# Kernel optimization log

Measured on AMD Instinct MI355X. Metric: run time of the kernel, lower is better.

Reference implementation:

```python
import jax, jax.numpy as jnp
import numpy as np

G = 200000
M = 9600000

def setup_inputs() -> dict:
    key = jax.random.key(0)
    k1, k2, k3, k4, k5, k6 = jax.random.split(key, 6)
    glimpse_feature = jax.random.normal(k1, (G, 256), dtype=jnp.float32)
    local_pos = jax.random.normal(k2, (M, 3), dtype=jnp.float32)
    log_mask = jax.random.normal(k3, (M, 1), dtype=jnp.float32)
    glimpse_index = jnp.sort(jax.random.randint(k4, (M,), 0, G))
    w = jax.random.normal(k5, (256, 1), dtype=jnp.float32) * 0.05
    b = jnp.zeros((1,), dtype=jnp.float32)
    noise = jnp.clip(jax.random.uniform(k6, (G,), dtype=jnp.float32), 1e-6, 1.0 - 1e-6)
    return {"glimpse_feature": glimpse_feature, "local_pos": local_pos,
            "log_mask": log_mask, "glimpse_index": glimpse_index,
            "w": w, "b": b, "noise": noise, "temperature": 1}

def reference(glimpse_feature, local_pos, log_mask, glimpse_index, w, b, noise, temperature):
    lm = log_mask[:, 0]                                    # [M]
    # scatter_log_softmax over segments
    seg_max = jax.ops.segment_max(lm, glimpse_index, num_segments=G)      # [G]
    shifted = lm - seg_max[glimpse_index]                                  # [M]
    seg_lse = jnp.log(jax.ops.segment_sum(jnp.exp(shifted), glimpse_index, num_segments=G))  # [G]
    norm_mask = jnp.exp(shifted - seg_lse[glimpse_index])[:, None]         # [M,1]
    # weighted scatter-sum -> per-glimpse member center
    member_center = jax.ops.segment_sum(local_pos * norm_mask, glimpse_index, num_segments=G)  # [G,3]
    # tiny Linear + tanh squashing
    logit_pres = 8.8 * jnp.tanh((glimpse_feature @ w + b)[:, 0])           # [G]
    # LogitRelaxedBernoulli rsample -> logsigmoid
    logistic = jnp.log(noise) - jnp.log1p(-noise)                          # [G]
    log_z_pres = jax.nn.log_sigmoid((logit_pres + logistic) / temperature)  # [G]
    return (log_z_pres, logit_pres, member_center)
```

## Files before the change

kernel.cpp:

```cpp
#include <hip/hip_runtime.h>
#include <math.h>

static constexpr int CHUNK = 8;
static constexpr int TPB   = 256;
static constexpr int MPB   = TPB * CHUNK;
static constexpr int LOCAL_BINS = 640;
static constexpr int ROWS_PER_BLOCK = 32;

__global__ __launch_bounds__(256)
void zero_ws_kernel(float4* __restrict__ ws, int n4) {
  int i = blockIdx.x * blockDim.x + threadIdx.x;
  int stride = gridDim.x * blockDim.x;
  for (; i < n4; i += stride) ws[i] = make_float4(0.f, 0.f, 0.f, 0.f);
}

__global__ __launch_bounds__(TPB)
void fused_kernel(const float* __restrict__ lm,
                  const float* __restrict__ pos,
                  const int*   __restrict__ idx,
                  const float* __restrict__ gf,
                  const float* __restrict__ w,
                  const float* __restrict__ bptr,
                  const float* __restrict__ noise,
                  const int*   __restrict__ temp_ptr,
                  float* __restrict__ seg_sum,
                  float* __restrict__ center_raw,
                  float* __restrict__ out,
                  int M, int G, int nseg, int ntot) {
  __shared__ float bins[LOCAL_BINS * 4];

  long long r = blockIdx.x;
  int segcum  = (int)((r * (long long)nseg) / ntot);
  int segcum1 = (int)(((r + 1) * (long long)nseg) / ntot);

  if (segcum1 != segcum) {
    int blockBase = segcum * MPB;
    if (blockBase >= M) return;
    int blockEnd = min(blockBase + MPB, M);
    int g_first = idx[blockBase];
    int g_last  = idx[blockEnd - 1];
    int span    = g_last - g_first + 1;
    int nbins   = min(span, LOCAL_BINS);

    for (int i = threadIdx.x; i < nbins * 4; i += TPB) bins[i] = 0.f;
    __syncthreads();

    int base = blockBase + threadIdx.x * CHUNK;
    if (base < M) {
      auto flush = [&](int g, float se, float sx, float sy, float sz) {
        int off = g - g_first;
        if (off < LOCAL_BINS) {
          unsafeAtomicAdd(&bins[off*4+0], se);
          unsafeAtomicAdd(&bins[off*4+1], sx);
          unsafeAtomicAdd(&bins[off*4+2], sy);
          unsafeAtomicAdd(&bins[off*4+3], sz);
        } else {
          unsafeAtomicAdd(&seg_sum[g], se);
          unsafeAtomicAdd(&center_raw[3*g+0], sx);
          unsafeAtomicAdd(&center_raw[3*g+1], sy);
          unsafeAtomicAdd(&center_raw[3*g+2], sz);
        }
      };

      if (base + CHUNK <= M) {
        const int4*   i4 = (const int4*)(idx + base);
        const float4* l4 = (const float4*)(lm + base);
        const float4* p4 = (const float4*)(pos + (size_t)base * 3);
        int4 ia = i4[0], ic = i4[1];
        float4 la = l4[0], lc = l4[1];
        float4 pA = p4[0], pB = p4[1], pC = p4[2],
               pD = p4[3], pE = p4[4], pF = p4[5];
        int   ib[CHUNK] = {ia.x,ia.y,ia.z,ia.w, ic.x,ic.y,ic.z,ic.w};
        float eb[CHUNK];
        eb[0]=__expf(la.x); eb[1]=__expf(la.y); eb[2]=__expf(la.z); eb[3]=__expf(la.w);
        eb[4]=__expf(lc.x); eb[5]=__expf(lc.y); eb[6]=__expf(lc.z); eb[7]=__expf(lc.w);
        float pb[CHUNK*3] = {pA.x,pA.y,pA.z,pA.w, pB.x,pB.y,pB.z,pB.w,
                             pC.x,pC.y,pC.z,pC.w, pD.x,pD.y,pD.z,pD.w,
                             pE.x,pE.y,pE.z,pE.w, pF.x,pF.y,pF.z,pF.w};

        if (ib[0] == ib[CHUNK-1]) {
          float se = 0.f, sx = 0.f, sy = 0.f, sz = 0.f;
          #pragma unroll
          for (int j = 0; j < CHUNK; j++) {
            se += eb[j];
            sx += pb[3*j+0] * eb[j];
            sy += pb[3*j+1] * eb[j];
            sz += pb[3*j+2] * eb[j];
          }
          flush(ib[0], se, sx, sy, sz);
        } else {
          int cur = ib[0];
          float se = 0.f, sx = 0.f, sy = 0.f, sz = 0.f;
          #pragma unroll
          for (int j = 0; j < CHUNK; j++) {
            if (ib[j] != cur) {
              flush(cur, se, sx, sy, sz);
              cur = ib[j]; se = 0.f; sx = 0.f; sy = 0.f; sz = 0.f;
            }
            se += eb[j];
            sx += pb[3*j+0] * eb[j];
            sy += pb[3*j+1] * eb[j];
            sz += pb[3*j+2] * eb[j];
          }
          flush(cur, se, sx, sy, sz);
        }
      } else {
        int nj = M - base;
        int cur = idx[base];
        float se = 0.f, sx = 0.f, sy = 0.f, sz = 0.f;
        for (int j = 0; j < nj; j++) {
          int g = idx[base + j];
          float e = __expf(lm[base + j]);
          if (g != cur) {
            flush(cur, se, sx, sy, sz);
            cur = g; se = 0.f; sx = 0.f; sy = 0.f; sz = 0.f;
          }
          se += e;
          sx += pos[(size_t)(base+j)*3+0] * e;
          sy += pos[(size_t)(base+j)*3+1] * e;
          sz += pos[(size_t)(base+j)*3+2] * e;
        }
        flush(cur, se, sx, sy, sz);
      }
    }
    __syncthreads();

    for (int i = threadIdx.x; i < nbins; i += TPB) {
      int g = g_first + i;
      float s0 = bins[i*4+0], s1 = bins[i*4+1], s2 = bins[i*4+2], s3 = bins[i*4+3];
      if (g == g_first || g == g_last) {
        unsafeAtomicAdd(&seg_sum[g], s0);
        unsafeAtomicAdd(&center_raw[3*g+0], s1);
        unsafeAtomicAdd(&center_raw[3*g+1], s2);
        unsafeAtomicAdd(&center_raw[3*g+2], s3);
      } else {
        seg_sum[g] = s0;
        center_raw[3*g+0] = s1;
        center_raw[3*g+1] = s2;
        center_raw[3*g+2] = s3;
      }
    }
  } else {
    int mb   = (int)(r - segcum);
    int wid  = threadIdx.x >> 6;
    int lane = threadIdx.x & 63;
    int sub  = lane & 15;
    int rg   = lane >> 4;

    int row0 = (mb * 4 + wid) * 8;
    int rowA = row0 + rg;
    int rowB = row0 + 4 + rg;

    const float4* w4 = (const float4*)w;
    float4 wv0 = w4[sub +  0], wv1 = w4[sub + 16],
           wv2 = w4[sub + 32], wv3 = w4[sub + 48];

    float dA = 0.f, dB = 0.f;
    if (rowA < G) {
      const float4* ga = (const float4*)(gf + (size_t)rowA * 256);
      const float4* gb = (const float4*)(gf + (size_t)rowB * 256);
      float4 a0 = ga[sub +  0], a1 = ga[sub + 16],
             a2 = ga[sub + 32], a3 = ga[sub + 48];
      float4 b0 = gb[sub +  0], b1 = gb[sub + 16],
             b2 = gb[sub + 32], b3 = gb[sub + 48];
      dA  = a0.x*wv0.x + a0.y*wv0.y + a0.z*wv0.z + a0.w*wv0.w;
      dA += a1.x*wv1.x + a1.y*wv1.y + a1.z*wv1.z + a1.w*wv1.w;
      dA += a2.x*wv2.x + a2.y*wv2.y + a2.z*wv2.z + a2.w*wv2.w;
      dA += a3.x*wv3.x + a3.y*wv3.y + a3.z*wv3.z + a3.w*wv3.w;
      dB  = b0.x*wv0.x + b0.y*wv0.y + b0.z*wv0.z + b0.w*wv0.w;
      dB += b1.x*wv1.x + b1.y*wv1.y + b1.z*wv1.z + b1.w*wv1.w;
      dB += b2.x*wv2.x + b2.y*wv2.y + b2.z*wv2.z + b2.w*wv2.w;
      dB += b3.x*wv3.x + b3.y*wv3.y + b3.z*wv3.z + b3.w*wv3.w;
    }
    #pragma unroll
    for (int m = 8; m >= 1; m >>= 1) {
      dA += __shfl_xor(dA, m, 64);
      dB += __shfl_xor(dB, m, 64);
    }

    if (sub == 0 && rowA < G) {
      float bb = bptr[0];
      int iv = temp_ptr[0];
      float tT = (iv > -(1 << 23) && iv < (1 << 23)) ? (float)iv : __int_as_float(iv);

      float logitA = 8.8f * tanhf(dA + bb);
      float nA = noise[rowA];
      float xA = (logitA + (logf(nA) - log1pf(-nA))) / tT;
      out[rowA]     = fminf(xA, 0.f) - log1pf(expf(-fabsf(xA)));
      out[G + rowA] = logitA;

      if (rowB < G) {
        float logitB = 8.8f * tanhf(dB + bb);
        float nB = noise[rowB];
        float xB = (logitB + (logf(nB) - log1pf(-nB))) / tT;
        out[rowB]     = fminf(xB, 0.f) - log1pf(expf(-fabsf(xB)));
        out[G + rowB] = logitB;
      }
    }
  }
}

__global__ __launch_bounds__(256)
void norm_kernel(const float* __restrict__ seg_sum,
                 const float* __restrict__ center_raw,
                 float* __restrict__ out, int G) {
  int i = blockIdx.x * blockDim.x + threadIdx.x;
  int n = 3 * G;
  if (i < n) {
    int g = i / 3;
    float s = seg_sum[g];
    float inv = (s > 0.f) ? (1.f / s) : 0.f;
    out[(size_t)2 * G + i] = center_raw[i] * inv;
  }
}

extern "C" void kernel_launch(void* const* d_in, const int* in_sizes, int n_in,
                              void* d_out, int out_size, void* d_ws, size_t ws_size,
                              hipStream_t stream) {
  const float* gf    = (const float*)d_in[0];
  const float* pos   = (const float*)d_in[1];
  const float* lm    = (const float*)d_in[2];
  const int*   idx   = (const int*)  d_in[3];
  const float* w     = (const float*)d_in[4];
  const float* b     = (const float*)d_in[5];
  const float* noise = (const float*)d_in[6];
  const int*   temp  = (const int*)  d_in[7];
  float* out = (float*)d_out;

  int G = in_sizes[6];
  int M = in_sizes[3];

  float* seg_sum    = (float*)d_ws;
  float* center_raw = seg_sum + G;

  int n4 = (4 * G) / 4;
  hipLaunchKernelGGL(zero_ws_kernel, dim3(784), dim3(256), 0, stream,
                     (float4*)d_ws, n4);

  int nseg = (M + MPB - 1) / MPB;
  int nmlp = (G + ROWS_PER_BLOCK - 1) / ROWS_PER_BLOCK;
  int ntot = nseg + nmlp;
  hipLaunchKernelGGL(fused_kernel, dim3(ntot), dim3(TPB), 0, stream,
                     lm, pos, idx, gf, w, b, noise, temp,
                     seg_sum, center_raw, out, M, G, nseg, ntot);

  int nblk = (3 * G + 255) / 256;
  hipLaunchKernelGGL(norm_kernel, dim3(nblk), dim3(256), 0, stream,
                     seg_sum, center_raw, out, G);
}
```

Baseline: 96.10 us.

## Stage position loads through padded LDS for coalesced per-wave access

Each wave now loads its 256-member slice of positions as contiguous float4s into a padded LDS staging buffer and then reads back per-lane triples. Indices and log-masks are also read as one coalesced int4/float4 per lane. Each thread now handles 4 members per pass over two passes instead of 8 strided members. The aim is fully coalesced global reads in place of per-thread 96-byte strided loads. The cost is extra LDS traffic, fewer local bins (448), and reliance on inline s_waitcnt asm rather than a barrier for intra-wave visibility.

After: 113.0 us. +17.6%, slower.

```diff
diff --git a/kernel.cpp b/kernel.cpp
--- a/kernel.cpp
+++ b/kernel.cpp
@@ -1,10 +1,12 @@
 #include <hip/hip_runtime.h>
 #include <math.h>
 
-static constexpr int CHUNK = 8;
 static constexpr int TPB   = 256;
-static constexpr int MPB   = TPB * CHUNK;
-static constexpr int LOCAL_BINS = 640;
+static constexpr int MPB   = 2048;
+static constexpr int WMEM  = 512;
+static constexpr int PMEM  = 256;
+static constexpr int LOCAL_BINS = 448;
+static constexpr int STAGE_F4   = 200;
 static constexpr int ROWS_PER_BLOCK = 32;
 
 __global__ __launch_bounds__(256)
@@ -27,7 +29,8 @@
                   float* __restrict__ center_raw,
                   float* __restrict__ out,
                   int M, int G, int nseg, int ntot) {
-  __shared__ float bins[LOCAL_BINS * 4];
+  __shared__ float  bins[LOCAL_BINS * 4];
+  __shared__ float4 stage[4][STAGE_F4];
 
   long long r = blockIdx.x;
   int segcum  = (int)((r * (long long)nseg) / ntot);
@@ -45,83 +48,99 @@
     for (int i = threadIdx.x; i < nbins * 4; i += TPB) bins[i] = 0.f;
     __syncthreads();
 
-    int base = blockBase + threadIdx.x * CHUNK;
-    if (base < M) {
-      auto flush = [&](int g, float se, float sx, float sy, float sz) {
-        int off = g - g_first;
-        if (off < LOCAL_BINS) {
-          unsafeAtomicAdd(&bins[off*4+0], se);
-          unsafeAtomicAdd(&bins[off*4+1], sx);
-          unsafeAtomicAdd(&bins[off*4+2], sy);
-          unsafeAtomicAdd(&bins[off*4+3], sz);
+    int wid  = threadIdx.x >> 6;
+    int lane = threadIdx.x & 63;
+
+    auto flush = [&](int g, float se, float sx, float sy, float sz) {
+      int off = g - g_first;
+      if (off < LOCAL_BINS) {
+        unsafeAtomicAdd(&bins[off*4+0], se);
+        unsafeAtomicAdd(&bins[off*4+1], sx);
+        unsafeAtomicAdd(&bins[off*4+2], sy);
+        unsafeAtomicAdd(&bins[off*4+3], sz);
+      } else {
+        unsafeAtomicAdd(&seg_sum[g], se);
+        unsafeAtomicAdd(&center_raw[3*g+0], sx);
+        unsafeAtomicAdd(&center_raw[3*g+1], sy);
+        unsafeAtomicAdd(&center_raw[3*g+2], sz);
+      }
+    };
+
+    #pragma unroll
+    for (int h = 0; h < 2; h++) {
+      int memBase = blockBase + wid * WMEM + h * PMEM;
+      if (memBase < M) {
+        if (memBase + PMEM <= M) {
+          const float4* p4 = (const float4*)(pos + (size_t)memBase * 3);
+          #pragma unroll
+          for (int k = 0; k < 3; k++) {
+            int j = lane + 64 * k;
+            stage[wid][j + j / 24] = p4[j];
+          }
+          const int4*   i4 = (const int4*)(idx + memBase);
+          const float4* l4 = (const float4*)(lm + memBase);
+          int4   ib = i4[lane];
+          float4 lv = l4[lane];
+          asm volatile("s_waitcnt lgkmcnt(0)" ::: "memory");
+          int j0 = 3 * lane;
+          float4 s0 = stage[wid][j0     +  j0      / 24];
+          float4 s1 = stage[wid][j0 + 1 + (j0 + 1) / 24];
+          float4 s2 = stage[wid][j0 + 2 + (j0 + 2) / 24];
+
+          float eb[4];
+          eb[0] = __expf(lv.x); eb[1] = __expf(lv.y);
+          eb[2] = __expf(lv.z); eb[3] = __expf(lv.w);
+          int   ibv[4] = {ib.x, ib.y, ib.z, ib.w};
+          float px[4] = {s0.x, s0.w, s1.z, s2.y};
+          float py[4] = {s0.y, s1.x, s1.w, s2.z};
+          float pz[4] = {s0.z, s1.y, s2.x, s2.w};
+
+          if (ib.x == ib.w) {
+            float se = eb[0]+eb[1]+eb[2]+eb[3];
+            float sx = px[0]*eb[0]+px[1]*eb[1]+px[2]*eb[2]+px[3]*eb[3];
+            float sy = py[0]*eb[0]+py[1]*eb[1]+py[2]*eb[2]+py[3]*eb[3];
+            float sz = pz[0]*eb[0]+pz[1]*eb[1]+pz[2]*eb[2]+pz[3]*eb[3];
+            flush(ib.x, se, sx, sy, sz);
+          } else {
+            int cur = ibv[0];
+            float se = 0.f, sx = 0.f, sy = 0.f, sz = 0.f;
+            #pragma unroll
+            for (int j = 0; j < 4; j++) {
+              if (ibv[j] != cur) {
+                flush(cur, se, sx, sy, sz);
+                cur = ibv[j]; se = 0.f; sx = 0.f; sy = 0.f; sz = 0.f;
+              }
+              se += eb[j];
+              sx += px[j] * eb[j];
+              sy += py[j] * eb[j];
+              sz += pz[j] * eb[j];
+            }
+            flush(cur, se, sx, sy, sz);
+          }
         } else {
-          unsafeAtomicAdd(&seg_sum[g], se);
-          unsafeAtomicAdd(&center_raw[3*g+0], sx);
-          unsafeAtomicAdd(&center_raw[3*g+1], sy);
-          unsafeAtomicAdd(&center_raw[3*g+2], sz);
+          int mstart = memBase + 4 * lane;
+          if (mstart < M) {
+            int nj = min(4, M - mstart);
+            int cur = idx[mstart];
+            float se = 0.f, sx = 0.f, sy = 0.f, sz = 0.f;
+            for (int j = 0; j < nj; j++) {
+              int m = mstart + j;
+              int g = idx[m];
+              float e = __expf(lm[m]);
+              if (g != cur) {
+                flush(cur, se, sx, sy, sz);
+                cur = g; se = 0.f; sx = 0.f; sy = 0.f; sz = 0.f;
+              }
+              se += e;
+              sx += pos[(size_t)m*3+0] * e;
+              sy += pos[(size_t)m*3+1] * e;
+              sz += pos[(size_t)m*3+2] * e;
+            }
+            flush(cur, se, sx, sy, sz);
+          }
         }
-      };
-
-      if (base + CHUNK <= M) {
-        const int4*   i4 = (const int4*)(idx + base);
-        const float4* l4 = (const float4*)(lm + base);
-        const float4* p4 = (const float4*)(pos + (size_t)base * 3);
-        int4 ia = i4[0], ic = i4[1];
-        float4 la = l4[0], lc = l4[1];
-        float4 pA = p4[0], pB = p4[1], pC = p4[2],
-               pD = p4[3], pE = p4[4], pF = p4[5];
-        int   ib[CHUNK] = {ia.x,ia.y,ia.z,ia.w, ic.x,ic.y,ic.z,ic.w};
-        float eb[CHUNK];
-        eb[0]=__expf(la.x); eb[1]=__expf(la.y); eb[2]=__expf(la.z); eb[3]=__expf(la.w);
-        eb[4]=__expf(lc.x); eb[5]=__expf(lc.y); eb[6]=__expf(lc.z); eb[7]=__expf(lc.w);
-        float pb[CHUNK*3] = {pA.x,pA.y,pA.z,pA.w, pB.x,pB.y,pB.z,pB.w,
-                             pC.x,pC.y,pC.z,pC.w, pD.x,pD.y,pD.z,pD.w,
-                             pE.x,pE.y,pE.z,pE.w, pF.x,pF.y,pF.z,pF.w};
-
-        if (ib[0] == ib[CHUNK-1]) {
-          float se = 0.f, sx = 0.f, sy = 0.f, sz = 0.f;
-          #pragma unroll
-          for (int j = 0; j < CHUNK; j++) {
-            se += eb[j];
-            sx += pb[3*j+0] * eb[j];
-            sy += pb[3*j+1] * eb[j];
-            sz += pb[3*j+2] * eb[j];
-          }
-          flush(ib[0], se, sx, sy, sz);
-        } else {
-          int cur = ib[0];
-          float se = 0.f, sx = 0.f, sy = 0.f, sz = 0.f;
-          #pragma unroll
-          for (int j = 0; j < CHUNK; j++) {
-            if (ib[j] != cur) {
-              flush(cur, se, sx, sy, sz);
-              cur = ib[j]; se = 0.f; sx = 0.f; sy = 0.f; sz = 0.f;
-            }
-            se += eb[j];
-            sx += pb[3*j+0] * eb[j];
-            sy += pb[3*j+1] * eb[j];
-            sz += pb[3*j+2] * eb[j];
-          }
-          flush(cur, se, sx, sy, sz);
-        }
-      } else {
-        int nj = M - base;
-        int cur = idx[base];
-        float se = 0.f, sx = 0.f, sy = 0.f, sz = 0.f;
-        for (int j = 0; j < nj; j++) {
-          int g = idx[base + j];
-          float e = __expf(lm[base + j]);
-          if (g != cur) {
-            flush(cur, se, sx, sy, sz);
-            cur = g; se = 0.f; sx = 0.f; sy = 0.f; sz = 0.f;
-          }
-          se += e;
-          sx += pos[(size_t)(base+j)*3+0] * e;
-          sy += pos[(size_t)(base+j)*3+1] * e;
-          sz += pos[(size_t)(base+j)*3+2] * e;
-        }
-        flush(cur, se, sx, sy, sz);
-      }
+      }
+      asm volatile("" ::: "memory");
     }
     __syncthreads();
 
```
